# Performance work log

Hardware: AMD Instinct MI355X
Metric: run time of the kernel (lower is better)

## Reference

```python
import jax, jax.numpy as jnp
import numpy as np

B, RES, STRIDE = 256, 14, 2
IN_DIM, OUT_DIM, KEY_DIM, HEADS, ATTN_RATIO = 384, 512, 16, 12, 2.0
VAL_DIM = int(ATTN_RATIO * KEY_DIM)            # 32
KEY_ATTN = KEY_DIM * HEADS                     # 192
VAL_ATTN = VAL_DIM * HEADS                     # 384
KV_DIM = KEY_ATTN + VAL_ATTN                   # 576
N = RES * RES                                  # 196
NQ = ((RES - 1) // STRIDE + 1) ** 2            # 49
SCALE = KEY_DIM ** -0.5
BN_EPS = 1e-5


def _bias_idxs():
    ki, kj = np.meshgrid(np.arange(RES), np.arange(RES), indexing='ij')
    k_pos = np.stack([ki.ravel(), kj.ravel()])                 # (2, N)
    qi, qj = np.meshgrid(np.arange(0, RES, STRIDE), np.arange(0, RES, STRIDE), indexing='ij')
    q_pos = np.stack([qi.ravel(), qj.ravel()])                 # (2, NQ)
    rel = np.abs(q_pos[:, :, None] - k_pos[:, None, :])        # (2, NQ, N)
    return jnp.asarray(rel[0] * RES + rel[1], dtype=jnp.int32) # (NQ, N)


def setup_inputs() -> dict:
    key = jax.random.key(0)
    ks = jax.random.split(key, 20)
    f = jax.random.normal
    u = lambda k, s: jax.random.uniform(k, s, jnp.float32, 0.5, 1.5)
    return {
        'x': f(ks[0], (B, N, IN_DIM), jnp.float32),
        'kv_w': f(ks[1], (KV_DIM, IN_DIM), jnp.float32) * 0.05,
        'kv_g': u(ks[2], (KV_DIM,)), 'kv_b': f(ks[3], (KV_DIM,)) * 0.1,
        'kv_m': f(ks[4], (KV_DIM,)) * 0.1, 'kv_v': u(ks[5], (KV_DIM,)),
        'q_w': f(ks[6], (KEY_ATTN, IN_DIM), jnp.float32) * 0.05,
        'q_g': u(ks[7], (KEY_ATTN,)), 'q_b': f(ks[8], (KEY_ATTN,)) * 0.1,
        'q_m': f(ks[9], (KEY_ATTN,)) * 0.1, 'q_v': u(ks[10], (KEY_ATTN,)),
        'pj_w': f(ks[11], (OUT_DIM, VAL_ATTN), jnp.float32) * 0.05,
        'pj_g': u(ks[12], (OUT_DIM,)), 'pj_b': f(ks[13], (OUT_DIM,)) * 0.1,
        'pj_m': f(ks[14], (OUT_DIM,)) * 0.1, 'pj_v': u(ks[15], (OUT_DIM,)),
        'biases': f(ks[16], (HEADS, N), jnp.float32) * 0.1,
        'bias_idxs': _bias_idxs(),
    }


def _bn(x, g, b, m, v):
    # BatchNorm (eval mode, running stats), affine
    return (x - m) * (g * jax.lax.rsqrt(v + BN_EPS)) + b


def reference(x, kv_w, kv_g, kv_b, kv_m, kv_v,
              q_w, q_g, q_b, q_m, q_v,
              pj_w, pj_g, pj_b, pj_m, pj_v,
              biases, bias_idxs):
    Bsz, Nn, C = x.shape
    # kv = LinearNorm(x): (B, N, KV_DIM)
    kv = _bn(jnp.einsum('bnc,dc->bnd', x, kv_w), kv_g, kv_b, kv_m, kv_v)
    kv = kv.reshape(Bsz, Nn, HEADS, KEY_DIM + VAL_DIM)
    k = kv[..., :KEY_DIM].transpose(0, 2, 3, 1)   # (B, H, KD, N)
    v = kv[..., KEY_DIM:].transpose(0, 2, 1, 3)   # (B, H, N, VD)
    # q path: strided spatial downsample then LinearNorm
    xq = x.reshape(Bsz, RES, RES, C)[:, ::STRIDE, ::STRIDE].reshape(Bsz, -1, C)  # (B, NQ, C)
    q = _bn(jnp.einsum('bnc,dc->bnd', xq, q_w), q_g, q_b, q_m, q_v)
    q = q.reshape(Bsz, NQ, HEADS, KEY_DIM).transpose(0, 2, 1, 3)  # (B, H, NQ, KD)
    # gathered relative-position bias: (H, NQ, N)
    attn_bias = biases[:, bias_idxs]
    attn = jnp.einsum('bhqd,bhdk->bhqk', q, k) * SCALE + attn_bias
    attn = jax.nn.softmax(attn, axis=-1)
    out = jnp.einsum('bhqk,bhkd->bhqd', attn, v)                  # (B, H, NQ, VD)
    out = out.transpose(0, 2, 1, 3).reshape(Bsz, NQ, VAL_ATTN)
    # proj: SiLU -> LinearNorm
    out = jax.nn.silu(out)
    out = _bn(jnp.einsum('bnc,dc->bnd', out, pj_w), pj_g, pj_b, pj_m, pj_v)
    return out
```

## Files before the change

### kernel.cpp

```cpp
#include <hip/hip_runtime.h>
#include <hip/hip_bf16.h>


typedef __bf16 bf16;
typedef float f32x4 __attribute__((ext_vector_type(4)));
typedef __bf16 bf16x8 __attribute__((ext_vector_type(8)));
typedef __bf16 bf16x4 __attribute__((ext_vector_type(4)));

#define KV2_BLK 18816
#define KV2_VOFF 6272
#define Q2_BLK 1568
#define LOG2E 1.4426950408889634f
#define QSCALE 0.36067376022224085f

__device__ __forceinline__ void gl2lds16(const bf16* g, bf16* l) {
  __builtin_amdgcn_global_load_lds(
      (const __attribute__((address_space(1))) void*)g,
      (__attribute__((address_space(3))) void*)l, 16, 0, 0);
}

__global__ void cast_kernel(const float* __restrict__ src, bf16* __restrict__ dst, long n) {
  long i = ((long)blockIdx.x * 256 + threadIdx.x) * 8;
  if (i + 8 <= n) {
    f32x4 lo = *(const f32x4*)(src + i), hi = *(const f32x4*)(src + i + 4);
    bf16x8 t;
    t[0]=(bf16)lo[0]; t[1]=(bf16)lo[1]; t[2]=(bf16)lo[2]; t[3]=(bf16)lo[3];
    t[4]=(bf16)hi[0]; t[5]=(bf16)hi[1]; t[6]=(bf16)hi[2]; t[7]=(bf16)hi[3];
    *(bf16x8*)(dst + i) = t;
  }
}

__global__ void wcast_kernel(const float* __restrict__ kv_w, const float* __restrict__ q_w,
                             const float* __restrict__ pj_w, bf16* __restrict__ kvwb,
                             bf16* __restrict__ qwb, bf16* __restrict__ pjwb) {
  long i = ((long)blockIdx.x * 256 + threadIdx.x) * 8;
  const float* s; bf16* d; long off;
  if (i < 221184)      { s = kv_w; d = kvwb; off = 0; }
  else if (i < 294912) { s = q_w;  d = qwb;  off = 221184; }
  else if (i < 491520) { s = pj_w; d = pjwb; off = 294912; }
  else return;
  long j = i - off;
  f32x4 lo = *(const f32x4*)(s + j), hi = *(const f32x4*)(s + j + 4);
  bf16x8 t;
  t[0]=(bf16)lo[0]; t[1]=(bf16)lo[1]; t[2]=(bf16)lo[2]; t[3]=(bf16)lo[3];
  t[4]=(bf16)hi[0]; t[5]=(bf16)hi[1]; t[6]=(bf16)hi[2]; t[7]=(bf16)hi[3];
  *(bf16x8*)(d + j) = t;
}

__global__ void prep_kernel(const float* kv_g, const float* kv_b, const float* kv_m, const float* kv_v,
                            const float* q_g,  const float* q_b,  const float* q_m,  const float* q_v,
                            const float* p_g,  const float* p_b,  const float* p_m,  const float* p_v,
                            float* scbuf) {
  int i = blockIdx.x * 256 + threadIdx.x;
  const float *g, *bb, *mm, *vv;
  float *sc, *sh;
  int c;
  float f = 1.0f;
  if (i < 576)        { c = i;       g = kv_g; bb = kv_b; mm = kv_m; vv = kv_v; sc = scbuf;        sh = scbuf + 576;  }
  else if (i < 768)   { c = i - 576; g = q_g;  bb = q_b;  mm = q_m;  vv = q_v;  sc = scbuf + 1152; sh = scbuf + 1344; f = QSCALE; }
  else if (i < 1280)  { c = i - 768; g = p_g;  bb = p_b;  mm = p_m;  vv = p_v;  sc = scbuf + 1536; sh = scbuf + 2048; }
  else return;
  float sv = g[c] * rsqrtf(vv[c] + 1e-5f);
  sc[c] = sv * f;
  sh[c] = (bb[c] - mm[c] * sv) * f;
}

__global__ void bias_kernel(const float* biases, const int* idxs, float* biasp) {
  int i = blockIdx.x * 256 + threadIdx.x;
  if (i < 12 * 49 * 196) {
    int h = i / (49 * 196);
    int rem = i - h * (49 * 196);
    biasp[i] = biases[h * 196 + idxs[rem]] * LOG2E;
  }
}

template<int EPI, bool GATHER>
__global__ __launch_bounds__(128)
void gemm_bn_kernel(const bf16* __restrict__ A, const bf16* __restrict__ W,
                    const float* __restrict__ sc, const float* __restrict__ sh,
                    char* __restrict__ out, int N) {
  __shared__ __attribute__((aligned(16))) bf16 As[128 * 32];
  __shared__ __attribute__((aligned(16))) bf16 Ws[64 * 32];
  const int tid  = threadIdx.x;
  const int lane = tid & 63;
  const int wid  = tid >> 6;
  const int m0 = blockIdx.x * 128;
  const int n0 = blockIdx.y * 64;
  const int rquad = lane >> 2;
  const int kslot = lane & 3;

  long gA[4]; int lA[4];
#pragma unroll
  for (int i = 0; i < 4; ++i) {
    int rt = wid * 64 + i * 16 + rquad;
    long arow;
    if (GATHER) {
      int m = m0 + rt;
      int b = m / 49;
      int qq = m - b * 49;
      arow = (long)b * 196 + (qq / 7) * 28 + (qq % 7) * 2;
    } else {
      arow = m0 + rt;
    }
    gA[i] = arow * 384 + kslot * 8;
    lA[i] = (wid * 64 + i * 16) * 32;
  }
  long gW[2]; int lW[2];
#pragma unroll
  for (int j = 0; j < 2; ++j) {
    int rt = wid * 32 + j * 16 + rquad;
    gW[j] = (long)(n0 + rt) * 384 + kslot * 8;
    lW[j] = (wid * 32 + j * 16) * 32;
  }

  f32x4 acc[4][4] = {};
  const int mrow = lane & 15;
  const int quad = lane >> 4;

  for (int k0 = 0; k0 < 384; k0 += 32) {
#pragma unroll
    for (int i = 0; i < 4; ++i) gl2lds16(A + gA[i] + k0, As + lA[i]);
#pragma unroll
    for (int j = 0; j < 2; ++j) gl2lds16(W + gW[j] + k0, Ws + lW[j]);
    __syncthreads();

    bf16x8 af[4], bw[4];
#pragma unroll
    for (int mi = 0; mi < 4; ++mi)
      af[mi] = *(const bf16x8*)(As + (wid * 64 + mi * 16 + mrow) * 32 + quad * 8);
#pragma unroll
    for (int ni = 0; ni < 4; ++ni)
      bw[ni] = *(const bf16x8*)(Ws + (ni * 16 + mrow) * 32 + quad * 8);
#pragma unroll
    for (int mi = 0; mi < 4; ++mi)
#pragma unroll
      for (int ni = 0; ni < 4; ++ni)
        acc[mi][ni] = __builtin_amdgcn_mfma_f32_16x16x32_bf16(af[mi], bw[ni], acc[mi][ni], 0, 0, 0);
    __syncthreads();
  }

#pragma unroll
  for (int ni = 0; ni < 4; ++ni) {
    int col = n0 + ni * 16 + mrow;
    float s = sc[col], t = sh[col];
    int h = 0, dd = 0;
    if (EPI == 1) { h = col / 48; dd = col - h * 48; }
    if (EPI == 2) { h = col >> 4; dd = col & 15; }
#pragma unroll
    for (int mi = 0; mi < 4; ++mi) {
      int mbase = m0 + wid * 64 + mi * 16 + quad * 4;
      if (EPI == 0) {
#pragma unroll
        for (int reg = 0; reg < 4; ++reg) {
          int m = mbase + reg;
          ((float*)out)[(long)m * N + col] = acc[mi][ni][reg] * s + t;
        }
      } else if (EPI == 1) {
        int b = mbase / 196, j = mbase - b * 196;
        char* base = out + ((long)(b * 12 + h)) * KV2_BLK;
        if (dd < 16) {
#pragma unroll
          for (int reg = 0; reg < 4; ++reg)
            ((bf16*)base)[(j + reg) * 16 + dd] = (bf16)(acc[mi][ni][reg] * s + t);
        } else {
          bf16x4 tv;
#pragma unroll
          for (int reg = 0; reg < 4; ++reg)
            tv[reg] = (bf16)(acc[mi][ni][reg] * s + t);
          *(bf16x4*)((bf16*)(base + KV2_VOFF) + (dd - 16) * 196 + j) = tv;
        }
      } else {
#pragma unroll
        for (int reg = 0; reg < 4; ++reg) {
          int m = mbase + reg;
          int b = m / 49, qq = m - b * 49;
          ((bf16*)(out + ((long)(b * 12 + h)) * Q2_BLK))[qq * 16 + dd] = (bf16)(acc[mi][ni][reg] * s + t);
        }
      }
    }
  }
}

__global__ __launch_bounds__(256)
void attn_kernel(const char* __restrict__ kv2, const char* __restrict__ qb2,
                 const float* __restrict__ biasp, bf16* __restrict__ aout) {
  __shared__ __attribute__((aligned(16))) char smem[40448];
  bf16* vT_s = (bf16*)smem;
  bf16* k_s  = (bf16*)(smem + 12800);
  bf16* P_s  = (bf16*)(smem + 12800);

  const int bh = blockIdx.x;
  const int b = bh / 12;
  const int h = bh - b * 12;
  const int tid  = threadIdx.x;
  const int lane = tid & 63;
  const int wid  = tid >> 6;
  const int mrow = lane & 15;
  const int quad = lane >> 4;

  const bf16* ksrc = (const bf16*)(kv2 + (long)bh * KV2_BLK);
  const bf16* vsrc = (const bf16*)(kv2 + (long)bh * KV2_BLK + KV2_VOFF);
  const bf16* qsrc = (const bf16*)(qb2 + (long)bh * Q2_BLK);

  bf16x8 z = {};
  {
    for (int i = tid; i < 832; i += 256) {
      int r = i >> 2, c = i & 3;
      *(bf16x8*)(k_s + r * 40 + c * 8) =
          (r < 196 && c < 2) ? *(const bf16x8*)(ksrc + r * 16 + c * 8) : z;
    }
    bf16x4 z4 = {};
    for (int i = tid; i < 1600; i += 256) {
      int r = i / 50, c = i - r * 50;
      *(bf16x4*)(vT_s + r * 200 + c * 4) =
          (c < 49) ? *(const bf16x4*)(vsrc + r * 196 + c * 4) : z4;
    }
  }
  const int qrow = wid * 16 + mrow;
  bf16x8 aq = (quad < 2 && qrow < 49)
                  ? *(const bf16x8*)(qsrc + qrow * 16 + quad * 8) : z;
  __syncthreads();

  f32x4 s[13];
#pragma unroll
  for (int jt = 0; jt < 13; ++jt) {
    bf16x8 bk = *(const bf16x8*)(k_s + (jt * 16 + mrow) * 40 + quad * 8);
    f32x4 zz = {};
    s[jt] = __builtin_amdgcn_mfma_f32_16x16x32_bf16(aq, bk, zz, 0, 0, 0);
  }

  const int rbase = wid * 16 + quad * 4;
#pragma unroll
  for (int jt = 0; jt < 13; ++jt) {
    int c = jt * 16 + mrow;
#pragma unroll
    for (int reg = 0; reg < 4; ++reg) {
      int r = rbase + reg;
      float v = s[jt][reg];
      if (c < 196) {
        if (r < 49) v += biasp[((long)h * 49 + r) * 196 + c];
      } else {
        v = -1e30f;
      }
      s[jt][reg] = v;
    }
  }
  float mx[4], sm[4];
#pragma unroll
  for (int reg = 0; reg < 4; ++reg) {
    float m = -1e30f;
#pragma unroll
    for (int jt = 0; jt < 13; ++jt) m = fmaxf(m, s[jt][reg]);
    m = fmaxf(m, __shfl_xor(m, 1));
    m = fmaxf(m, __shfl_xor(m, 2));
    m = fmaxf(m, __shfl_xor(m, 4));
    m = fmaxf(m, __shfl_xor(m, 8));
    mx[reg] = m;
  }
#pragma unroll
  for (int jt = 0; jt < 13; ++jt) {
    int c = jt * 16 + mrow;
#pragma unroll
    for (int reg = 0; reg < 4; ++reg)
      s[jt][reg] = (c < 196) ? __builtin_amdgcn_exp2f(s[jt][reg] - mx[reg]) : 0.0f;
  }
#pragma unroll
  for (int reg = 0; reg < 4; ++reg) {
    float t = 0.0f;
#pragma unroll
    for (int jt = 0; jt < 13; ++jt) t += s[jt][reg];
    t += __shfl_xor(t, 1);
    t += __shfl_xor(t, 2);
    t += __shfl_xor(t, 4);
    t += __shfl_xor(t, 8);
    sm[reg] = 1.0f / t;
  }

  __syncthreads();

  bf16* Pw = P_s + wid * 16 * 216;
#pragma unroll
  for (int jt = 0; jt < 13; ++jt) {
#pragma unroll
    for (int reg = 0; reg < 4; ++reg)
      Pw[(quad * 4 + reg) * 216 + jt * 16 + mrow] = (bf16)(s[jt][reg] * sm[reg]);
  }

  f32x4 o[2] = {};
#pragma unroll
  for (int kk = 0; kk < 6; ++kk) {
    bf16x8 ap = *(const bf16x8*)(Pw + mrow * 216 + kk * 32 + quad * 8);
#pragma unroll
    for (int nt = 0; nt < 2; ++nt) {
      bf16x8 bv = *(const bf16x8*)(vT_s + (nt * 16 + mrow) * 200 + kk * 32 + quad * 8);
      o[nt] = __builtin_amdgcn_mfma_f32_16x16x32_bf16(ap, bv, o[nt], 0, 0, 0);
    }
  }
  {
    bf16x8 ap = (quad == 0) ? *(const bf16x8*)(Pw + mrow * 216 + 192) : z;
#pragma unroll
    for (int nt = 0; nt < 2; ++nt) {
      bf16x8 bv = (quad == 0) ? *(const bf16x8*)(vT_s + (nt * 16 + mrow) * 200 + 192) : z;
      o[nt] = __builtin_amdgcn_mfma_f32_16x16x32_bf16(ap, bv, o[nt], 0, 0, 0);
    }
  }

#pragma unroll
  for (int nt = 0; nt < 2; ++nt) {
#pragma unroll
    for (int reg = 0; reg < 4; ++reg) {
      int r = rbase + reg;
      if (r < 49) {
        float x = o[nt][reg];
        float sil = x / (1.0f + __expf(-x));
        aout[((long)b * 49 + r) * 384 + h * 32 + nt * 16 + mrow] = (bf16)sil;
      }
    }
  }
}

extern "C" void kernel_launch(void* const* d_in, const int* in_sizes, int n_in,
                              void* d_out, int out_size, void* d_ws, size_t ws_size,
                              hipStream_t stream) {
  const float* x      = (const float*)d_in[0];
  const float* kv_w   = (const float*)d_in[1];
  const float* q_w    = (const float*)d_in[6];
  const float* pj_w   = (const float*)d_in[11];
  const float* biases = (const float*)d_in[16];
  const int*   bidx   = (const int*)d_in[17];

  char* ws = (char*)d_ws;
  float* scbuf = (float*)ws;
  float* biasp = (float*)(ws + 10256);
  char*  qb2   = ws + 471296;
  bf16*  aout  = (bf16*)(ws + 5288192);
  bf16*  xb    = (bf16*)(ws + 14921984);
  bf16*  kvwb  = (bf16*)(ws + 53457152);
  bf16*  qwb   = (bf16*)(ws + 53899520);
  bf16*  pjwb  = (bf16*)(ws + 54046976);
  char*  kv2   = ws + 54440192;

  cast_kernel<<<9408, 256, 0, stream>>>(x, xb, 19267584L);
  wcast_kernel<<<240, 256, 0, stream>>>(kv_w, q_w, pj_w, kvwb, qwb, pjwb);

  prep_kernel<<<5, 256, 0, stream>>>(
      (const float*)d_in[2],  (const float*)d_in[3],  (const float*)d_in[4],  (const float*)d_in[5],
      (const float*)d_in[7],  (const float*)d_in[8],  (const float*)d_in[9],  (const float*)d_in[10],
      (const float*)d_in[12], (const float*)d_in[13], (const float*)d_in[14], (const float*)d_in[15],
      scbuf);
  bias_kernel<<<451, 256, 0, stream>>>(biases, bidx, biasp);

  gemm_bn_kernel<2, true><<<dim3(98, 3), 128, 0, stream>>>(
      xb, qwb, scbuf + 1152, scbuf + 1344, qb2, 192);

  gemm_bn_kernel<1, false><<<dim3(392, 9), 128, 0, stream>>>(
      xb, kvwb, scbuf, scbuf + 576, kv2, 576);

  attn_kernel<<<3072, 256, 0, stream>>>(kv2, qb2, biasp, aout);

  gemm_bn_kernel<0, false><<<dim3(98, 8), 128, 0, stream>>>(
      aout, pjwb, scbuf + 1536, scbuf + 2048, (char*)d_out, 512);
}
```

Measured before the change: 309.9 us.

## Pre-layout bias in MFMA fragment order and feed it as accumulator init

The bias table is now precomputed directly in the MFMA accumulator register layout, with the padding mask (-1e30) and the invalid rows folded in. The attention kernel loads it with coalesced 16-byte loads and uses it as the C operand of the QK MFMA, which removes the scattered per-element bias gathers and mask branches. Softmax normalization is deferred to after the PV product, and launch bounds request 4 blocks per SM. In exchange it holds 52 extra registers for the bias fragments, which may pressure occupancy.

```diff
diff --git a/kernel.cpp b/kernel.cpp
--- a/kernel.cpp
+++ b/kernel.cpp
@@ -65,13 +65,27 @@
   sh[c] = (bb[c] - mm[c] * sv) * f;
 }
 
-__global__ void bias_kernel(const float* biases, const int* idxs, float* biasp) {
+__global__ void bias_kernel(const float* biases, const int* idxs, float* biasp2) {
   int i = blockIdx.x * 256 + threadIdx.x;
-  if (i < 12 * 49 * 196) {
-    int h = i / (49 * 196);
-    int rem = i - h * (49 * 196);
-    biasp[i] = biases[h * 196 + idxs[rem]] * LOG2E;
-  }
+  if (i >= 39936) return;
+  int lane = i & 63;
+  int jt   = (i >> 6) % 13;
+  int hw   = i / (13 * 64);
+  int wid  = hw & 3;
+  int h    = hw >> 2;
+  int mrow = lane & 15, quad = lane >> 4;
+  int c = jt * 16 + mrow;
+  f32x4 v;
+#pragma unroll
+  for (int reg = 0; reg < 4; ++reg) {
+    int r = wid * 16 + quad * 4 + reg;
+    float val;
+    if (c >= 196)      val = -1e30f;
+    else if (r < 49)   val = biases[h * 196 + idxs[r * 196 + c]] * LOG2E;
+    else               val = 0.0f;
+    v[reg] = val;
+  }
+  ((f32x4*)biasp2)[i] = v;
 }
 
 template<int EPI, bool GATHER>
@@ -181,9 +195,9 @@
   }
 }
 
-__global__ __launch_bounds__(256)
+__global__ __launch_bounds__(256, 4)
 void attn_kernel(const char* __restrict__ kv2, const char* __restrict__ qb2,
-                 const float* __restrict__ biasp, bf16* __restrict__ aout) {
+                 const float* __restrict__ biasp2, bf16* __restrict__ aout) {
   __shared__ __attribute__((aligned(16))) char smem[40448];
   bf16* vT_s = (bf16*)smem;
   bf16* k_s  = (bf16*)(smem + 12800);
@@ -203,6 +217,16 @@
   const bf16* qsrc = (const bf16*)(qb2 + (long)bh * Q2_BLK);
 
   bf16x8 z = {};
+  const int qrow = wid * 16 + mrow;
+  bf16x8 aq = (quad < 2 && qrow < 49)
+                  ? *(const bf16x8*)(qsrc + qrow * 16 + quad * 8) : z;
+  f32x4 cb[13];
+  {
+    const f32x4* bf2 = (const f32x4*)biasp2 + ((long)(h * 4 + wid) * 13 * 64 + lane);
+#pragma unroll
+    for (int jt = 0; jt < 13; ++jt) cb[jt] = bf2[jt * 64];
+  }
+
   {
     for (int i = tid; i < 832; i += 256) {
       int r = i >> 2, c = i & 3;
@@ -216,35 +240,16 @@
           (c < 49) ? *(const bf16x4*)(vsrc + r * 196 + c * 4) : z4;
     }
   }
-  const int qrow = wid * 16 + mrow;
-  bf16x8 aq = (quad < 2 && qrow < 49)
-                  ? *(const bf16x8*)(qsrc + qrow * 16 + quad * 8) : z;
   __syncthreads();
 
   f32x4 s[13];
 #pragma unroll
   for (int jt = 0; jt < 13; ++jt) {
     bf16x8 bk = *(const bf16x8*)(k_s + (jt * 16 + mrow) * 40 + quad * 8);
-    f32x4 zz = {};
-    s[jt] = __builtin_amdgcn_mfma_f32_16x16x32_bf16(aq, bk, zz, 0, 0, 0);
+    s[jt] = __builtin_amdgcn_mfma_f32_16x16x32_bf16(aq, bk, cb[jt], 0, 0, 0);
   }
 
   const int rbase = wid * 16 + quad * 4;
-#pragma unroll
-  for (int jt = 0; jt < 13; ++jt) {
-    int c = jt * 16 + mrow;
-#pragma unroll
-    for (int reg = 0; reg < 4; ++reg) {
-      int r = rbase + reg;
-      float v = s[jt][reg];
-      if (c < 196) {
-        if (r < 49) v += biasp[((long)h * 49 + r) * 196 + c];
-      } else {
-        v = -1e30f;
-      }
-      s[jt][reg] = v;
-    }
-  }
   float mx[4], sm[4];
 #pragma unroll
   for (int reg = 0; reg < 4; ++reg) {
@@ -258,12 +263,10 @@
     mx[reg] = m;
   }
 #pragma unroll
-  for (int jt = 0; jt < 13; ++jt) {
-    int c = jt * 16 + mrow;
+  for (int jt = 0; jt < 13; ++jt)
 #pragma unroll
     for (int reg = 0; reg < 4; ++reg)
-      s[jt][reg] = (c < 196) ? __builtin_amdgcn_exp2f(s[jt][reg] - mx[reg]) : 0.0f;
-  }
+      s[jt][reg] = __builtin_amdgcn_exp2f(s[jt][reg] - mx[reg]);
 #pragma unroll
   for (int reg = 0; reg < 4; ++reg) {
     float t = 0.0f;
@@ -283,7 +286,7 @@
   for (int jt = 0; jt < 13; ++jt) {
 #pragma unroll
     for (int reg = 0; reg < 4; ++reg)
-      Pw[(quad * 4 + reg) * 216 + jt * 16 + mrow] = (bf16)(s[jt][reg] * sm[reg]);
+      Pw[(quad * 4 + reg) * 216 + jt * 16 + mrow] = (bf16)s[jt][reg];
   }
 
   f32x4 o[2] = {};
@@ -311,7 +314,7 @@
     for (int reg = 0; reg < 4; ++reg) {
       int r = rbase + reg;
       if (r < 49) {
-        float x = o[nt][reg];
+        float x = o[nt][reg] * sm[reg];
         float sil = x / (1.0f + __expf(-x));
         aout[((long)b * 49 + r) * 384 + h * 32 + nt * 16 + mrow] = (bf16)sil;
       }
@@ -331,7 +334,6 @@
 
   char* ws = (char*)d_ws;
   float* scbuf = (float*)ws;
-  float* biasp = (float*)(ws + 10256);
   char*  qb2   = ws + 471296;
   bf16*  aout  = (bf16*)(ws + 5288192);
   bf16*  xb    = (bf16*)(ws + 14921984);
@@ -339,6 +341,7 @@
   bf16*  qwb   = (bf16*)(ws + 53899520);
   bf16*  pjwb  = (bf16*)(ws + 54046976);
   char*  kv2   = ws + 54440192;
+  float* biasp2= (float*)(ws + 112242944);
 
   cast_kernel<<<9408, 256, 0, stream>>>(x, xb, 19267584L);
   wcast_kernel<<<240, 256, 0, stream>>>(kv_w, q_w, pj_w, kvwb, qwb, pjwb);
@@ -348,7 +351,7 @@
       (const float*)d_in[7],  (const float*)d_in[8],  (const float*)d_in[9],  (const float*)d_in[10],
       (const float*)d_in[12], (const float*)d_in[13], (const float*)d_in[14], (const float*)d_in[15],
       scbuf);
-  bias_kernel<<<451, 256, 0, stream>>>(biases, bidx, biasp);
+  bias_kernel<<<156, 256, 0, stream>>>(biases, bidx, biasp2);
 
   gemm_bn_kernel<2, true><<<dim3(98, 3), 128, 0, stream>>>(
       xb, qwb, scbuf + 1152, scbuf + 1344, qb2, 192);
@@ -356,7 +359,7 @@
   gemm_bn_kernel<1, false><<<dim3(392, 9), 128, 0, stream>>>(
       xb, kvwb, scbuf, scbuf + 576, kv2, 576);
 
-  attn_kernel<<<3072, 256, 0, stream>>>(kv2, qb2, biasp, aout);
+  attn_kernel<<<3072, 256, 0, stream>>>(kv2, qb2, biasp2, aout);
 
   gemm_bn_kernel<0, false><<<dim3(98, 8), 128, 0, stream>>>(
       aout, pjwb, scbuf + 1536, scbuf + 2048, (char*)d_out, 512);
```

New measurement: 277.4 us. 10.5% less time.
